# Kernel optimization log

Measured on AMD Instinct MI355X. Metric: run time of the kernel, lower is better.

Reference implementation:

```python
import jax, jax.numpy as jnp
import numpy as np

D = 768        # d_model
F = 8192       # dict_size
N_UP = 3       # number of upstream autoencoders
K = 64         # topk
B, S = 2, 1024


def setup_inputs() -> dict:
    key = jax.random.key(0)
    ks = jax.random.split(key, 10)
    sc = 1.0 / np.sqrt(D)
    return {
        "feature_buffer": jnp.zeros((B, S, F), jnp.float32),
        "x": jax.random.normal(ks[0], (B, S, D), jnp.float32),
        "up_feats": jax.random.uniform(ks[1], (N_UP, B, S, F), jnp.float32),
        "W_enc": jax.random.normal(ks[2], (D, F), jnp.float32) * sc,
        "b_enc": jax.random.normal(ks[3], (F,), jnp.float32) * 0.01,
        "W_dec": jax.random.normal(ks[4], (F, D), jnp.float32) * sc,
        "b_dec": jax.random.normal(ks[5], (D,), jnp.float32) * 0.01,
        "up_W_dec": jax.random.normal(ks[6], (N_UP, F, D), jnp.float32) * sc,
        "up_b_dec": jax.random.normal(ks[7], (N_UP, D), jnp.float32) * 0.01,
        "conn_mask": jax.random.randint(ks[8], (N_UP, F, F), 0, 2).astype(bool),
        "k": K,
    }


def reference(feature_buffer, x, up_feats, W_enc, b_enc, W_dec, b_dec,
              up_W_dec, up_b_dec, conn_mask, k):
    # initial contribs: residual stream through current encoder
    approx = jnp.einsum("bsd,df->bsf", x, W_enc)            # [B,S,F]
    upstream_bias = jnp.zeros((D,), x.dtype)
    # accumulate pruned contributions from each upstream AE
    for i in range(up_feats.shape[0]):
        upstream_bias = upstream_bias + up_b_dec[i]
        # virtual weights up_dict -> down_dict, pruned by connection mask
        virt = (up_W_dec[i] @ W_enc) * conn_mask[i].astype(x.dtype)  # [F_up,F_down]
        approx = approx + jnp.einsum("bsf,fg->bsg", up_feats[i], virt)
    # bias correction: upstream decoder biases through encoder, plus encoder bias
    approx = approx + upstream_bias @ W_enc + b_enc          # [B,S,F]
    # topk + relu + scatter into the feature buffer
    top_vals, top_idx = jax.lax.top_k(approx, k)             # [B,S,k]
    top_vals = jax.nn.relu(top_vals)
    flat = feature_buffer.reshape(-1, F)
    rows = jnp.arange(flat.shape[0])[:, None]
    feat = flat.at[rows, top_idx.reshape(-1, k)].set(top_vals.reshape(-1, k))
    feat = feat.reshape(feature_buffer.shape)
    # decode
    return jnp.einsum("bsf,fd->bsd", feat, W_dec) + b_dec
```

## Files before the change

### kernel.cpp

```cpp
#include <hip/hip_runtime.h>
#include <hip/hip_bf16.h>


#define D_DIM 768
#define F_DIM 8192

typedef _Float16 f16;
typedef _Float16 f16x8 __attribute__((ext_vector_type(8)));
typedef float f32x4 __attribute__((ext_vector_type(4)));

#define BMN 128
#define BUFB 32768
#define PLNB 16384

__device__ inline void split_f32(float v, f16& h, f16& l) {
    float hf = (float)(f16)v;
    if (__builtin_fabsf(hf) < 6.1035156e-5f) hf = 0.f;
    h = (f16)hf;
    l = (f16)((v - hf) * 2048.0f);
}

template<int MODE>
__global__ __launch_bounds__(256, 2)
void mfma_gemm(const f16* __restrict__ Ap,
               const f16* __restrict__ Bp,
               float* __restrict__ C, int ldc,
               f16* __restrict__ Vp,
               const float* __restrict__ bias,
               const unsigned char* __restrict__ conn, int upIdx,
               const int* __restrict__ flagp,
               int K, int fdBase)
{
    __shared__ char lds[2 * BUFB];
    const int tid = threadIdx.x;
    const int bm = (MODE == 2 ? blockIdx.x : blockIdx.y) * BMN;
    const int bn = (MODE == 2 ? blockIdx.y : blockIdx.x) * BMN;

    const int w  = tid >> 6;
    const int l  = tid & 63;
    const int wr = (w >> 1) * 64;
    const int wc = (w & 1) * 64;

    const char* gsrc[8];
    #pragma unroll
    for (int j = 0; j < 8; ++j) {
        const int c = tid + 256 * j;
        const int p = c >> 10;
        const int q = c & 1023;
        const int r = q >> 3;
        const int sp = q & 7;
        const int slog = sp ^ (r & 7);
        const f16* base = p ? Bp : Ap;
        const int row0 = p ? bn : bm;
        gsrc[j] = (const char*)base + (size_t)(row0 + r) * ((size_t)K * 4)
                  + slog * 16;
    }

    #define STAGE(BUFSEL)                                                     \
        _Pragma("unroll")                                                     \
        for (int j = 0; j < 8; ++j) {                                         \
            __builtin_amdgcn_global_load_lds(                                 \
                (const __attribute__((address_space(1))) void*)gsrc[j],       \
                (__attribute__((address_space(3))) void*)                     \
                    (lds + (BUFSEL) * BUFB + (tid + 256 * j) * 16),           \
                16, 0, 0);                                                    \
            gsrc[j] += 128;                       \
        }

    f32x4 accH[4][4], accM[4][4];
    const f32x4 zero = {0.f, 0.f, 0.f, 0.f};
    #pragma unroll
    for (int a = 0; a < 4; ++a)
        #pragma unroll
        for (int b = 0; b < 4; ++b) { accH[a][b] = zero; accM[a][b] = zero; }

    const int steps = K >> 5;
    const int fr = l & 15;
    const int ks = l >> 4;

    int offAH[4], offBH[4], offAL[4], offBL[4];
    #pragma unroll
    for (int f = 0; f < 4; ++f) {
        const int ra = wr + f * 16 + fr;
        const int rb = wc + f * 16 + fr;
        offAH[f] = ra * 128 + ((ks ^ (ra & 7)) * 16);
        offAL[f] = ra * 128 + (((4 + ks) ^ (ra & 7)) * 16);
        offBH[f] = PLNB + rb * 128 + ((ks ^ (rb & 7)) * 16);
        offBL[f] = PLNB + rb * 128 + (((4 + ks) ^ (rb & 7)) * 16);
    }

    STAGE(0);
    int cur = 0;
    for (int t = 0; t < steps; ++t) {
        __builtin_amdgcn_s_barrier();
        if (t + 1 < steps) {
            STAGE(cur ^ 1);
            asm volatile("s_waitcnt vmcnt(8)" ::: "memory");
        } else {
            asm volatile("s_waitcnt vmcnt(0)" ::: "memory");
        }
        __builtin_amdgcn_s_barrier();
        __builtin_amdgcn_sched_barrier(0);

        const char* Lb = lds + cur * BUFB;
        f16x8 ah[4], bh[4];
        #pragma unroll
        for (int mf = 0; mf < 4; ++mf) ah[mf] = *(const f16x8*)(Lb + offAH[mf]);
        #pragma unroll
        for (int nf = 0; nf < 4; ++nf) bh[nf] = *(const f16x8*)(Lb + offBH[nf]);

        f16x8 al[4], bl[4];
        #pragma unroll
        for (int nf = 0; nf < 4; ++nf) bl[nf] = *(const f16x8*)(Lb + offBL[nf]);
        #pragma unroll
        for (int mf = 0; mf < 4; ++mf) al[mf] = *(const f16x8*)(Lb + offAL[mf]);

        __builtin_amdgcn_s_setprio(1);
        #pragma unroll
        for (int nf = 0; nf < 4; ++nf)
            #pragma unroll
            for (int mf = 0; mf < 4; ++mf)
                accH[mf][nf] = __builtin_amdgcn_mfma_f32_16x16x32_f16(
                    ah[mf], bh[nf], accH[mf][nf], 0, 0, 0);
        __builtin_amdgcn_s_setprio(0);

        __builtin_amdgcn_s_setprio(1);
        #pragma unroll
        for (int nf = 0; nf < 4; ++nf)
            #pragma unroll
            for (int mf = 0; mf < 4; ++mf)
                accM[mf][nf] = __builtin_amdgcn_mfma_f32_16x16x32_f16(
                    ah[mf], bl[nf], accM[mf][nf], 0, 0, 0);
        #pragma unroll
        for (int mf = 0; mf < 4; ++mf)
            #pragma unroll
            for (int nf = 0; nf < 4; ++nf)
                accM[mf][nf] = __builtin_amdgcn_mfma_f32_16x16x32_f16(
                    al[mf], bh[nf], accM[mf][nf], 0, 0, 0);
        __builtin_amdgcn_s_setprio(0);

        cur ^= 1;
    }
    #undef STAGE

    const float MS = 4.8828125e-4f;
    const int flag = (MODE == 1) ? *flagp : 0;

    #pragma unroll
    for (int mf = 0; mf < 4; ++mf) {
        const int row0 = wr + mf * 16 + (l >> 4) * 4;
        #pragma unroll
        for (int nf = 0; nf < 4; ++nf) {
            const int col = wc + nf * 16 + (l & 15);
            float v[4];
            #pragma unroll
            for (int rr = 0; rr < 4; ++rr)
                v[rr] = accH[mf][nf][rr] + accM[mf][nf][rr] * MS;

            if (MODE == 0) {
                const float bb = bias[bn + col];
                #pragma unroll
                for (int rr = 0; rr < 4; ++rr)
                    C[(size_t)(bm + row0 + rr) * ldc + (bn + col)] = v[rr] + bb;
            } else if (MODE == 2) {
                #pragma unroll
                for (int rr = 0; rr < 4; ++rr) {
                    float* cp = &C[(size_t)(bm + row0 + rr) * ldc + (bn + col)];
                    *cp = *cp + v[rr];
                }
            } else {
                const size_t fu = (size_t)(bn + col);
                const size_t fd0 = (size_t)(fdBase + bm + row0);
                int m[4];
                if (flag == 1) {
                    const int4 mm = *(const int4*)((const int*)conn +
                        (size_t)upIdx * F_DIM * F_DIM + fu * F_DIM + fd0);
                    m[0] = mm.x; m[1] = mm.y; m[2] = mm.z; m[3] = mm.w;
                } else if (flag == 0) {
                    const uchar4 mm = *(const uchar4*)(conn +
                        (size_t)upIdx * F_DIM * F_DIM + fu * F_DIM + fd0);
                    m[0] = mm.x; m[1] = mm.y; m[2] = mm.z; m[3] = mm.w;
                } else if (flag == 2) {
                    const long long* pp = (const long long*)conn +
                        (size_t)upIdx * F_DIM * F_DIM + fu * F_DIM + fd0;
                    m[0] = (int)pp[0]; m[1] = (int)pp[1];
                    m[2] = (int)pp[2]; m[3] = (int)pp[3];
                } else {
                    const float4 mm = *(const float4*)((const float*)conn +
                        (size_t)upIdx * F_DIM * F_DIM + fu * F_DIM + fd0);
                    m[0] = mm.x != 0.f; m[1] = mm.y != 0.f;
                    m[2] = mm.z != 0.f; m[3] = mm.w != 0.f;
                }
                const size_t kblk = (fu >> 5) * 64 + (fu & 31);
                #pragma unroll
                for (int rr = 0; rr < 4; ++rr) {
                    const float vv = m[rr] ? v[rr] : 0.f;
                    f16 hh, ll;
                    split_f32(vv, hh, ll);
                    const size_t o = (size_t)(bm + row0 + rr) * (2 * F_DIM) + kblk;
                    Vp[o] = hh; Vp[o + 32] = ll;
                }
            }
        }
    }
}

__global__ __launch_bounds__(256)
void split_kernel(const float* __restrict__ src, f16* __restrict__ dst,
                  size_t n, int K)
{
    const size_t e = ((size_t)blockIdx.x * 256 + threadIdx.x) * 8;
    if (e >= n) return;
    const size_t r = e / (size_t)K;
    const int k = (int)(e - r * (size_t)K);
    const float4 a = *(const float4*)(src + e);
    const float4 b = *(const float4*)(src + e + 4);
    f16 hv[8], lv[8];
    const float s[8] = {a.x, a.y, a.z, a.w, b.x, b.y, b.z, b.w};
    #pragma unroll
    for (int i = 0; i < 8; ++i) split_f32(s[i], hv[i], lv[i]);
    const size_t base = r * (size_t)(2 * K) + (size_t)((k >> 5) * 64 + (k & 31));
    *(f16x8*)(dst + base)      = *(const f16x8*)hv;
    *(f16x8*)(dst + base + 32) = *(const f16x8*)lv;
}

__global__ __launch_bounds__(256)
void transpose_split_kernel(const float* __restrict__ W, f16* __restrict__ dst)
{
    const int f = blockIdx.x * 256 + threadIdx.x;
    for (int dc = 0; dc < D_DIM / 8; ++dc) {
        const int k = dc * 8;
        f16 hv[8], lv[8];
        #pragma unroll
        for (int j = 0; j < 8; ++j)
            split_f32(W[(size_t)(k + j) * F_DIM + f], hv[j], lv[j]);
        const size_t base = (size_t)f * (2 * D_DIM) + (k >> 5) * 64 + (k & 31);
        *(f16x8*)(dst + base)      = *(const f16x8*)hv;
        *(f16x8*)(dst + base + 32) = *(const f16x8*)lv;
    }
}

__global__ void detect_kernel(const int* __restrict__ conn, int* __restrict__ flag)
{
    __shared__ int not01, notf01, odd_nz;
    if (threadIdx.x == 0) { not01 = 0; notf01 = 0; odd_nz = 0; }
    __syncthreads();
    const int4 v = ((const int4*)conn)[threadIdx.x];
    const unsigned a[4] = {(unsigned)v.x, (unsigned)v.y,
                           (unsigned)v.z, (unsigned)v.w};
    int l_not01 = 0, l_notf = 0;
    #pragma unroll
    for (int i = 0; i < 4; ++i) {
        if (a[i] > 1u) l_not01 = 1;
        if (a[i] != 0u && a[i] != 0x3F800000u) l_notf = 1;
    }
    if (l_not01) atomicOr(&not01, 1);
    if (l_notf)  atomicOr(&notf01, 1);
    if (a[1] | a[3]) atomicOr(&odd_nz, 1);
    __syncthreads();
    if (threadIdx.x == 0) {
        int f;
        if (!not01)        f = odd_nz ? 1 : 2;
        else if (!notf01)  f = 3;
        else               f = 0;
        *flag = f;
    }
}

__global__ void bias2_kernel(const float* __restrict__ W_enc,
                             const float* __restrict__ b_enc,
                             const float* __restrict__ up_b_dec,
                             int nup, float* __restrict__ bias2)
{
    const int g = blockIdx.x * 256 + threadIdx.x;
    if (g >= F_DIM) return;
    float s = b_enc[g];
    for (int d = 0; d < D_DIM; ++d) {
        float ub = 0.f;
        for (int i = 0; i < nup; ++i) ub += up_b_dec[i * D_DIM + d];
        s = __builtin_fmaf(ub, W_enc[(size_t)d * F_DIM + g], s);
    }
    bias2[g] = s;
}

__global__ __launch_bounds__(256)
void topk_decode_kernel(const float* __restrict__ approx,
                        const float* __restrict__ W_dec,
                        const float* __restrict__ b_dec,
                        const int* __restrict__ kptr,
                        float* __restrict__ out)
{
    __shared__ unsigned keys[F_DIM];
    __shared__ int hist[256];
    __shared__ unsigned sh_prefix;
    __shared__ int sh_need;
    __shared__ int sel_cnt, eq_cnt;
    __shared__ int sidx[128];
    __shared__ float sval[128];
    __shared__ int eqidx[1024];

    const int tid = threadIdx.x;
    const int row = blockIdx.x;
    const int k = *kptr;
    const float* arow = approx + (size_t)row * F_DIM;

    for (int j = tid; j < F_DIM; j += 256) {
        unsigned u = __float_as_uint(arow[j]);
        u = (u & 0x80000000u) ? ~u : (u | 0x80000000u);
        keys[j] = u;
    }
    if (tid == 0) { sh_prefix = 0u; sh_need = k; sel_cnt = 0; eq_cnt = 0; }
    __syncthreads();

    for (int shift = 24; shift >= 0; shift -= 8) {
        if (tid < 256) hist[tid] = 0;
        __syncthreads();
        const unsigned pfx = sh_prefix;
        for (int j = tid; j < F_DIM; j += 256) {
            const unsigned u = keys[j];
            const bool match =
                (shift == 24) || ((u >> (shift + 8)) == (pfx >> (shift + 8)));
            if (match) atomicAdd(&hist[(u >> shift) & 255], 1);
        }
        __syncthreads();
        if (tid == 0) {
            int need = sh_need;
            for (int b = 255; b >= 0; --b) {
                const int c = hist[b];
                if (c >= need) {
                    sh_prefix = pfx | ((unsigned)b << shift);
                    sh_need = need;
                    break;
                }
                need -= c;
            }
        }
        __syncthreads();
    }
    const unsigned T = sh_prefix;
    const int r = sh_need;

    for (int j = tid; j < F_DIM; j += 256) {
        const unsigned u = keys[j];
        if (u > T) {
            const int p = atomicAdd(&sel_cnt, 1);
            sidx[p] = j;
        } else if (u == T) {
            const int p = atomicAdd(&eq_cnt, 1);
            if (p < 1024) eqidx[p] = j;
        }
    }
    __syncthreads();

    if (tid == 0) {
        const int m = sel_cnt;
        const int e = eq_cnt < 1024 ? eq_cnt : 1024;
        for (int t2 = 0; t2 < r; ++t2) {
            int best = 0x7FFFFFFF, bi = -1;
            for (int q = 0; q < e; ++q) {
                const int v = eqidx[q];
                if (v >= 0 && v < best) { best = v; bi = q; }
            }
            if (bi >= 0) { eqidx[bi] = -1; sidx[m + t2] = best; }
        }
        sel_cnt = m + r;
        const int n = sel_cnt;
        for (int a2 = 1; a2 < n; ++a2) {
            const int v = sidx[a2];
            int b2 = a2 - 1;
            while (b2 >= 0 && sidx[b2] > v) { sidx[b2 + 1] = sidx[b2]; --b2; }
            sidx[b2 + 1] = v;
        }
    }
    __syncthreads();

    const int total = sel_cnt;
    for (int j = tid; j < total; j += 256) {
        const float v = arow[sidx[j]];
        sval[j] = v > 0.f ? v : 0.f;
    }
    __syncthreads();

    float acc0 = b_dec[tid];
    float acc1 = b_dec[tid + 256];
    float acc2 = b_dec[tid + 512];
    for (int j = 0; j < total; ++j) {
        const float v = sval[j];
        const float* wv = W_dec + (size_t)sidx[j] * D_DIM;
        acc0 = __builtin_fmaf(v, wv[tid],       acc0);
        acc1 = __builtin_fmaf(v, wv[tid + 256], acc1);
        acc2 = __builtin_fmaf(v, wv[tid + 512], acc2);
    }
    float* orow = out + (size_t)row * D_DIM;
    orow[tid] = acc0;
    orow[tid + 256] = acc1;
    orow[tid + 512] = acc2;
}

extern "C" void kernel_launch(void* const* d_in, const int* in_sizes, int n_in,
                              void* d_out, int out_size, void* d_ws, size_t ws_size,
                              hipStream_t stream)
{
    const float* x         = (const float*)d_in[1];
    const float* up_feats  = (const float*)d_in[2];
    const float* W_enc     = (const float*)d_in[3];
    const float* b_enc     = (const float*)d_in[4];
    const float* W_dec     = (const float*)d_in[5];
    const float* b_dec     = (const float*)d_in[6];
    const float* up_W_dec  = (const float*)d_in[7];
    const float* up_b_dec  = (const float*)d_in[8];
    const unsigned char* conn = (const unsigned char*)d_in[9];
    const int* kptr        = (const int*)d_in[10];

    const int BS  = in_sizes[1] / D_DIM;
    const int NUP = in_sizes[8] / D_DIM;

    char* ws = (char*)d_ws;
    size_t off = 0;
    auto alloc = [&](size_t bytes) -> char* {
        off = (off + 255) & ~(size_t)255;
        char* p = ws + off; off += bytes; return p;
    };
    float* approx = (float*)alloc((size_t)BS * F_DIM * 4);
    float* bias2  = (float*)alloc(F_DIM * 4);
    int*   flag   = (int*)alloc(256);
    f16* xp   = (f16*)alloc((size_t)BS * D_DIM * 4);
    f16* Wtp  = (f16*)alloc((size_t)F_DIM * D_DIM * 4);
    f16* uwdp = (f16*)alloc((size_t)NUP * F_DIM * D_DIM * 4);
    f16* ufp  = (f16*)alloc((size_t)NUP * BS * F_DIM * 4);

    off = (off + 255) & ~(size_t)255;
    const size_t rem = (ws_size > off) ? ws_size - off : 0;
    int FC = (int)((rem / ((size_t)F_DIM * 4)) / 128 * 128);
    if (FC > F_DIM) FC = F_DIM;
    if (FC < 128) FC = 128;
    f16* vp = (f16*)alloc((size_t)FC * F_DIM * 4);

    detect_kernel<<<1, 256, 0, stream>>>((const int*)conn, flag);
    bias2_kernel<<<F_DIM / 256, 256, 0, stream>>>(W_enc, b_enc, up_b_dec, NUP, bias2);

    split_kernel<<<(unsigned)((size_t)BS * D_DIM / 2048), 256, 0, stream>>>(
        x, xp, (size_t)BS * D_DIM, D_DIM);
    split_kernel<<<(unsigned)((size_t)NUP * F_DIM * D_DIM / 2048), 256, 0, stream>>>(
        up_W_dec, uwdp, (size_t)NUP * F_DIM * D_DIM, D_DIM);
    split_kernel<<<(unsigned)((size_t)NUP * BS * F_DIM / 2048), 256, 0, stream>>>(
        up_feats, ufp, (size_t)NUP * BS * F_DIM, F_DIM);
    transpose_split_kernel<<<F_DIM / 256, 256, 0, stream>>>(W_enc, Wtp);

    mfma_gemm<0><<<dim3(F_DIM / BMN, BS / BMN), 256, 0, stream>>>(
        xp, Wtp, approx, F_DIM, nullptr, bias2,
        nullptr, 0, flag, D_DIM, 0);

    for (int i = 0; i < NUP; ++i) {
        for (int fc = 0; fc < F_DIM; fc += FC) {
            const int chunk = (F_DIM - fc) < FC ? (F_DIM - fc) : FC;
            mfma_gemm<1><<<dim3(F_DIM / BMN, chunk / BMN), 256, 0, stream>>>(
                Wtp + (size_t)fc * (2 * D_DIM),
                uwdp + (size_t)i * F_DIM * (2 * D_DIM),
                nullptr, 0, vp, nullptr,
                conn, i, flag, D_DIM, fc);
            mfma_gemm<2><<<dim3(BS / BMN, chunk / BMN), 256, 0, stream>>>(
                ufp + (size_t)i * BS * (2 * F_DIM),
                vp,
                approx + fc, F_DIM, nullptr, nullptr,
                nullptr, 0, flag, F_DIM, 0);
        }
    }

    topk_decode_kernel<<<BS, 256, 0, stream>>>(
        approx, W_dec, b_dec, kptr, (float*)d_out);
}
```

Before: 3.855 ms.

## Load B fragments directly to registers and merge split-f16 accumulators

After: 5.985 ms. 55.2% more time.

```diff
diff --git a/kernel.cpp b/kernel.cpp
--- a/kernel.cpp
+++ b/kernel.cpp
@@ -10,8 +10,7 @@
 typedef float f32x4 __attribute__((ext_vector_type(4)));
 
 #define BMN 128
-#define BUFB 32768
-#define PLNB 16384
+#define BUFB 16384
 
 __device__ inline void split_f32(float v, f16& h, f16& l) {
     float hf = (float)(f16)v;
@@ -40,108 +39,128 @@
     const int l  = tid & 63;
     const int wr = (w >> 1) * 64;
     const int wc = (w & 1) * 64;
-
-    const char* gsrc[8];
-    #pragma unroll
-    for (int j = 0; j < 8; ++j) {
+    const int fr = l & 15;
+    const int ks = l >> 4;
+
+    const char* gA[4];
+    #pragma unroll
+    for (int j = 0; j < 4; ++j) {
         const int c = tid + 256 * j;
-        const int p = c >> 10;
-        const int q = c & 1023;
-        const int r = q >> 3;
-        const int sp = q & 7;
-        const int slog = sp ^ (r & 7);
-        const f16* base = p ? Bp : Ap;
-        const int row0 = p ? bn : bm;
-        gsrc[j] = (const char*)base + (size_t)(row0 + r) * ((size_t)K * 4)
-                  + slog * 16;
-    }
-
-    #define STAGE(BUFSEL)                                                     \
-        _Pragma("unroll")                                                     \
-        for (int j = 0; j < 8; ++j) {                                         \
+        const int r = c >> 3;
+        const int slog = (c & 7) ^ (r & 7);
+        gA[j] = (const char*)Ap + (size_t)(bm + r) * ((size_t)K * 4) + slog * 16;
+    }
+
+    const char* gBH[4];
+    const char* gBL[4];
+    #pragma unroll
+    for (int nf = 0; nf < 4; ++nf) {
+        const size_t row = (size_t)(bn + wc + nf * 16 + fr);
+        gBH[nf] = (const char*)Bp + row * ((size_t)K * 4) + ks * 16;
+        gBL[nf] = gBH[nf] + 64;
+    }
+
+    #define STAGE_A(BUFSEL)                                                   \
+        _Pragma("unroll")                                                     \
+        for (int j = 0; j < 4; ++j) {                                         \
             __builtin_amdgcn_global_load_lds(                                 \
-                (const __attribute__((address_space(1))) void*)gsrc[j],       \
+                (const __attribute__((address_space(1))) void*)gA[j],         \
                 (__attribute__((address_space(3))) void*)                     \
                     (lds + (BUFSEL) * BUFB + (tid + 256 * j) * 16),           \
                 16, 0, 0);                                                    \
-            gsrc[j] += 128;                       \
-        }
-
-    f32x4 accH[4][4], accM[4][4];
+            gA[j] += 128;                                                     \
+        }
+
+    #define LOADB(BH, BL)                                                     \
+        _Pragma("unroll")                                                     \
+        for (int nf = 0; nf < 4; ++nf) {                                      \
+            BH[nf] = *(const f16x8*)gBH[nf]; gBH[nf] += 128;                  \
+            BL[nf] = *(const f16x8*)gBL[nf]; gBL[nf] += 128;                  \
+        }
+
+    f32x4 acc[4][4];
     const f32x4 zero = {0.f, 0.f, 0.f, 0.f};
     #pragma unroll
     for (int a = 0; a < 4; ++a)
         #pragma unroll
-        for (int b = 0; b < 4; ++b) { accH[a][b] = zero; accM[a][b] = zero; }
+        for (int b = 0; b < 4; ++b) acc[a][b] = zero;
 
     const int steps = K >> 5;
-    const int fr = l & 15;
-    const int ks = l >> 4;
-
-    int offAH[4], offBH[4], offAL[4], offBL[4];
+
+    int offAH[4], offAL[4];
     #pragma unroll
     for (int f = 0; f < 4; ++f) {
         const int ra = wr + f * 16 + fr;
-        const int rb = wc + f * 16 + fr;
         offAH[f] = ra * 128 + ((ks ^ (ra & 7)) * 16);
         offAL[f] = ra * 128 + (((4 + ks) ^ (ra & 7)) * 16);
-        offBH[f] = PLNB + rb * 128 + ((ks ^ (rb & 7)) * 16);
-        offBL[f] = PLNB + rb * 128 + (((4 + ks) ^ (rb & 7)) * 16);
-    }
-
-    STAGE(0);
+    }
+
+    const f16 SC = (f16)2048.0f;
+
+    #define COMPUTE(BUFSEL, BH, BL)                                           \
+    {                                                                         \
+        const char* Lb = lds + (BUFSEL) * BUFB;                               \
+        f16x8 ah[4], al[4];                                                   \
+        _Pragma("unroll")                                                     \
+        for (int mf = 0; mf < 4; ++mf) ah[mf] = *(const f16x8*)(Lb + offAH[mf]); \
+        _Pragma("unroll")                                                     \
+        for (int mf = 0; mf < 4; ++mf) al[mf] = *(const f16x8*)(Lb + offAL[mf]); \
+        __builtin_amdgcn_s_setprio(1);                                        \
+        _Pragma("unroll")                                                     \
+        for (int nf = 0; nf < 4; ++nf)                                        \
+            _Pragma("unroll")                                                 \
+            for (int mf = 0; mf < 4; ++mf)                                    \
+                acc[mf][nf] = __builtin_amdgcn_mfma_f32_16x16x32_f16(         \
+                    ah[mf], BL[nf], acc[mf][nf], 0, 0, 0);                    \
+        __builtin_amdgcn_s_setprio(0);                                        \
+        _Pragma("unroll")                                                     \
+        for (int mf = 0; mf < 4; ++mf) ah[mf] = ah[mf] * SC;                  \
+        __builtin_amdgcn_s_setprio(1);                                        \
+        _Pragma("unroll")                                                     \
+        for (int nf = 0; nf < 4; ++nf)                                        \
+            _Pragma("unroll")                                                 \
+            for (int mf = 0; mf < 4; ++mf)                                    \
+                acc[mf][nf] = __builtin_amdgcn_mfma_f32_16x16x32_f16(         \
+                    ah[mf], BH[nf], acc[mf][nf], 0, 0, 0);                    \
+        _Pragma("unroll")                                                     \
+        for (int mf = 0; mf < 4; ++mf)                                        \
+            _Pragma("unroll")                                                 \
+            for (int nf = 0; nf < 4; ++nf)                                    \
+                acc[mf][nf] = __builtin_amdgcn_mfma_f32_16x16x32_f16(         \
+                    al[mf], BH[nf], acc[mf][nf], 0, 0, 0);                    \
+        __builtin_amdgcn_s_setprio(0);                                        \
+    }
+
+    f16x8 bhE[4], blE[4], bhO[4], blO[4];
+    STAGE_A(0);
+    LOADB(bhE, blE);
     int cur = 0;
-    for (int t = 0; t < steps; ++t) {
+    for (int t = 0; t < steps; t += 2) {
         __builtin_amdgcn_s_barrier();
-        if (t + 1 < steps) {
-            STAGE(cur ^ 1);
-            asm volatile("s_waitcnt vmcnt(8)" ::: "memory");
+        STAGE_A(cur ^ 1);
+        LOADB(bhO, blO);
+        asm volatile("s_waitcnt vmcnt(12)" ::: "memory");
+        __builtin_amdgcn_s_barrier();
+        __builtin_amdgcn_sched_barrier(0);
+        COMPUTE(cur, bhE, blE);
+        cur ^= 1;
+
+        __builtin_amdgcn_s_barrier();
+        if (t + 2 < steps) {
+            STAGE_A(cur ^ 1);
+            LOADB(bhE, blE);
+            asm volatile("s_waitcnt vmcnt(12)" ::: "memory");
         } else {
             asm volatile("s_waitcnt vmcnt(0)" ::: "memory");
         }
         __builtin_amdgcn_s_barrier();
         __builtin_amdgcn_sched_barrier(0);
-
-        const char* Lb = lds + cur * BUFB;
-        f16x8 ah[4], bh[4];
-        #pragma unroll
-        for (int mf = 0; mf < 4; ++mf) ah[mf] = *(const f16x8*)(Lb + offAH[mf]);
-        #pragma unroll
-        for (int nf = 0; nf < 4; ++nf) bh[nf] = *(const f16x8*)(Lb + offBH[nf]);
-
-        f16x8 al[4], bl[4];
-        #pragma unroll
-        for (int nf = 0; nf < 4; ++nf) bl[nf] = *(const f16x8*)(Lb + offBL[nf]);
-        #pragma unroll
-        for (int mf = 0; mf < 4; ++mf) al[mf] = *(const f16x8*)(Lb + offAL[mf]);
-
-        __builtin_amdgcn_s_setprio(1);
-        #pragma unroll
-        for (int nf = 0; nf < 4; ++nf)
-            #pragma unroll
-            for (int mf = 0; mf < 4; ++mf)
-                accH[mf][nf] = __builtin_amdgcn_mfma_f32_16x16x32_f16(
-                    ah[mf], bh[nf], accH[mf][nf], 0, 0, 0);
-        __builtin_amdgcn_s_setprio(0);
-
-        __builtin_amdgcn_s_setprio(1);
-        #pragma unroll
-        for (int nf = 0; nf < 4; ++nf)
-            #pragma unroll
-            for (int mf = 0; mf < 4; ++mf)
-                accM[mf][nf] = __builtin_amdgcn_mfma_f32_16x16x32_f16(
-                    ah[mf], bl[nf], accM[mf][nf], 0, 0, 0);
-        #pragma unroll
-        for (int mf = 0; mf < 4; ++mf)
-            #pragma unroll
-            for (int nf = 0; nf < 4; ++nf)
-                accM[mf][nf] = __builtin_amdgcn_mfma_f32_16x16x32_f16(
-                    al[mf], bh[nf], accM[mf][nf], 0, 0, 0);
-        __builtin_amdgcn_s_setprio(0);
-
+        COMPUTE(cur, bhO, blO);
         cur ^= 1;
     }
-    #undef STAGE
+    #undef COMPUTE
+    #undef LOADB
+    #undef STAGE_A
 
     const float MS = 4.8828125e-4f;
     const int flag = (MODE == 1) ? *flagp : 0;
@@ -155,7 +174,7 @@
             float v[4];
             #pragma unroll
             for (int rr = 0; rr < 4; ++rr)
-                v[rr] = accH[mf][nf][rr] + accM[mf][nf][rr] * MS;
+                v[rr] = acc[mf][nf][rr] * MS;
 
             if (MODE == 0) {
                 const float bb = bias[bn + col];
```

## Enlarge GEMM tiles to 256x256 with 8 waves and single split-fp16 accumulator

Applied to the files above, without the earlier changes.

Measured after the change: 3.997 ms. 3.7% more time.

```diff
diff --git a/kernel.cpp b/kernel.cpp
--- a/kernel.cpp
+++ b/kernel.cpp
@@ -9,9 +9,9 @@
 typedef _Float16 f16x8 __attribute__((ext_vector_type(8)));
 typedef float f32x4 __attribute__((ext_vector_type(4)));
 
-#define BMN 128
-#define BUFB 32768
-#define PLNB 16384
+#define BMN 256
+#define BUFB 65536
+#define PLNB 32768
 
 __device__ inline void split_f32(float v, f16& h, f16& l) {
     float hf = (float)(f16)v;
@@ -21,7 +21,7 @@
 }
 
 template<int MODE>
-__global__ __launch_bounds__(256, 2)
+__global__ __launch_bounds__(512, 2)
 void mfma_gemm(const f16* __restrict__ Ap,
                const f16* __restrict__ Bp,
                float* __restrict__ C, int ldc,
@@ -38,56 +38,61 @@
 
     const int w  = tid >> 6;
     const int l  = tid & 63;
-    const int wr = (w >> 1) * 64;
-    const int wc = (w & 1) * 64;
-
-    const char* gsrc[8];
-    #pragma unroll
-    for (int j = 0; j < 8; ++j) {
-        const int c = tid + 256 * j;
-        const int p = c >> 10;
-        const int q = c & 1023;
-        const int r = q >> 3;
-        const int sp = q & 7;
-        const int slog = sp ^ (r & 7);
-        const f16* base = p ? Bp : Ap;
-        const int row0 = p ? bn : bm;
-        gsrc[j] = (const char*)base + (size_t)(row0 + r) * ((size_t)K * 4)
-                  + slog * 16;
+    const int wr = (w >> 2) * 128;
+    const int wc = (w & 3) * 64;
+    const int fr = l & 15;
+    const int ks = l >> 4;
+
+    const char* gA[4];
+    const char* gB[4];
+    #pragma unroll
+    for (int j = 0; j < 4; ++j) {
+        const int c = tid + 512 * j;
+        const int r = c >> 3;
+        const int slog = (c & 7) ^ (r & 7);
+        gA[j] = (const char*)Ap + (size_t)(bm + r) * ((size_t)K * 4) + slog * 16;
+        gB[j] = (const char*)Bp + (size_t)(bn + r) * ((size_t)K * 4) + slog * 16;
     }
 
     #define STAGE(BUFSEL)                                                     \
         _Pragma("unroll")                                                     \
-        for (int j = 0; j < 8; ++j) {                                         \
+        for (int j = 0; j < 4; ++j) {                                         \
             __builtin_amdgcn_global_load_lds(                                 \
-                (const __attribute__((address_space(1))) void*)gsrc[j],       \
+                (const __attribute__((address_space(1))) void*)gA[j],         \
                 (__attribute__((address_space(3))) void*)                     \
-                    (lds + (BUFSEL) * BUFB + (tid + 256 * j) * 16),           \
+                    (lds + (BUFSEL) * BUFB + (tid + 512 * j) * 16),           \
                 16, 0, 0);                                                    \
-            gsrc[j] += 128;                       \
-        }
-
-    f32x4 accH[4][4], accM[4][4];
+            __builtin_amdgcn_global_load_lds(                                 \
+                (const __attribute__((address_space(1))) void*)gB[j],         \
+                (__attribute__((address_space(3))) void*)                     \
+                    (lds + (BUFSEL) * BUFB + PLNB + (tid + 512 * j) * 16),    \
+                16, 0, 0);                                                    \
+            gA[j] += 128;                                                     \
+            gB[j] += 128;                                                     \
+        }
+
+    f32x4 acc[8][4];
     const f32x4 zero = {0.f, 0.f, 0.f, 0.f};
     #pragma unroll
-    for (int a = 0; a < 4; ++a)
-        #pragma unroll
-        for (int b = 0; b < 4; ++b) { accH[a][b] = zero; accM[a][b] = zero; }
+    for (int a = 0; a < 8; ++a)
+        #pragma unroll
+        for (int b = 0; b < 4; ++b) acc[a][b] = zero;
 
     const int steps = K >> 5;
-    const int fr = l & 15;
-    const int ks = l >> 4;
-
-    int offAH[4], offBH[4], offAL[4], offBL[4];
+
+    int offAH[8], offBH[4];
+    #pragma unroll
+    for (int f = 0; f < 8; ++f) {
+        const int ra = wr + f * 16 + fr;
+        offAH[f] = ra * 128 + ((ks ^ (ra & 7)) * 16);
+    }
     #pragma unroll
     for (int f = 0; f < 4; ++f) {
-        const int ra = wr + f * 16 + fr;
         const int rb = wc + f * 16 + fr;
-        offAH[f] = ra * 128 + ((ks ^ (ra & 7)) * 16);
-        offAL[f] = ra * 128 + (((4 + ks) ^ (ra & 7)) * 16);
         offBH[f] = PLNB + rb * 128 + ((ks ^ (rb & 7)) * 16);
-        offBL[f] = PLNB + rb * 128 + (((4 + ks) ^ (rb & 7)) * 16);
-    }
+    }
+
+    const f16 SC = (f16)2048.0f;
 
     STAGE(0);
     int cur = 0;
@@ -103,40 +108,47 @@
         __builtin_amdgcn_sched_barrier(0);
 
         const char* Lb = lds + cur * BUFB;
-        f16x8 ah[4], bh[4];
-        #pragma unroll
-        for (int mf = 0; mf < 4; ++mf) ah[mf] = *(const f16x8*)(Lb + offAH[mf]);
-        #pragma unroll
-        for (int nf = 0; nf < 4; ++nf) bh[nf] = *(const f16x8*)(Lb + offBH[nf]);
-
-        f16x8 al[4], bl[4];
-        #pragma unroll
-        for (int nf = 0; nf < 4; ++nf) bl[nf] = *(const f16x8*)(Lb + offBL[nf]);
-        #pragma unroll
-        for (int mf = 0; mf < 4; ++mf) al[mf] = *(const f16x8*)(Lb + offAL[mf]);
+        f16x8 ah[8], bh[4], bl[4];
+        #pragma unroll
+        for (int mf = 0; mf < 8; ++mf) ah[mf] = *(const f16x8*)(Lb + offAH[mf]);
+        #pragma unroll
+        for (int nf = 0; nf < 4; ++nf) {
+            bh[nf] = *(const f16x8*)(Lb + offBH[nf]);
+            bl[nf] = *(const f16x8*)(Lb + (offBH[nf] ^ 64));
+        }
 
         __builtin_amdgcn_s_setprio(1);
         #pragma unroll
         for (int nf = 0; nf < 4; ++nf)
             #pragma unroll
-            for (int mf = 0; mf < 4; ++mf)
-                accH[mf][nf] = __builtin_amdgcn_mfma_f32_16x16x32_f16(
-                    ah[mf], bh[nf], accH[mf][nf], 0, 0, 0);
+            for (int mf = 0; mf < 8; ++mf)
+                acc[mf][nf] = __builtin_amdgcn_mfma_f32_16x16x32_f16(
+                    ah[mf], bl[nf], acc[mf][nf], 0, 0, 0);
         __builtin_amdgcn_s_setprio(0);
+
+        #pragma unroll
+        for (int mf = 0; mf < 8; ++mf) ah[mf] = ah[mf] * SC;
 
         __builtin_amdgcn_s_setprio(1);
         #pragma unroll
         for (int nf = 0; nf < 4; ++nf)
             #pragma unroll
-            for (int mf = 0; mf < 4; ++mf)
-                accM[mf][nf] = __builtin_amdgcn_mfma_f32_16x16x32_f16(
-                    ah[mf], bl[nf], accM[mf][nf], 0, 0, 0);
-        #pragma unroll
-        for (int mf = 0; mf < 4; ++mf)
+            for (int mf = 0; mf < 8; ++mf)
+                acc[mf][nf] = __builtin_amdgcn_mfma_f32_16x16x32_f16(
+                    ah[mf], bh[nf], acc[mf][nf], 0, 0, 0);
+        __builtin_amdgcn_s_setprio(0);
+
+        f16x8 al[8];
+        #pragma unroll
+        for (int mf = 0; mf < 8; ++mf)
+            al[mf] = *(const f16x8*)(Lb + (offAH[mf] ^ 64));
+        __builtin_amdgcn_s_setprio(1);
+        #pragma unroll
+        for (int mf = 0; mf < 8; ++mf)
             #pragma unroll
             for (int nf = 0; nf < 4; ++nf)
-                accM[mf][nf] = __builtin_amdgcn_mfma_f32_16x16x32_f16(
-                    al[mf], bh[nf], accM[mf][nf], 0, 0, 0);
+                acc[mf][nf] = __builtin_amdgcn_mfma_f32_16x16x32_f16(
+                    al[mf], bh[nf], acc[mf][nf], 0, 0, 0);
         __builtin_amdgcn_s_setprio(0);
 
         cur ^= 1;
@@ -147,7 +159,7 @@
     const int flag = (MODE == 1) ? *flagp : 0;
 
     #pragma unroll
-    for (int mf = 0; mf < 4; ++mf) {
+    for (int mf = 0; mf < 8; ++mf) {
         const int row0 = wr + mf * 16 + (l >> 4) * 4;
         #pragma unroll
         for (int nf = 0; nf < 4; ++nf) {
@@ -155,7 +167,7 @@
             float v[4];
             #pragma unroll
             for (int rr = 0; rr < 4; ++rr)
-                v[rr] = accH[mf][nf][rr] + accM[mf][nf][rr] * MS;
+                v[rr] = acc[mf][nf][rr] * MS;
 
             if (MODE == 0) {
                 const float bb = bias[bn + col];
@@ -431,9 +443,9 @@
 
     off = (off + 255) & ~(size_t)255;
     const size_t rem = (ws_size > off) ? ws_size - off : 0;
-    int FC = (int)((rem / ((size_t)F_DIM * 4)) / 128 * 128);
+    int FC = (int)((rem / ((size_t)F_DIM * 4)) / 256 * 256);
     if (FC > F_DIM) FC = F_DIM;
-    if (FC < 128) FC = 128;
+    if (FC < 256) FC = 256;
     f16* vp = (f16*)alloc((size_t)FC * F_DIM * 4);
 
     detect_kernel<<<1, 256, 0, stream>>>((const int*)conn, flag);
@@ -447,19 +459,19 @@
         up_feats, ufp, (size_t)NUP * BS * F_DIM, F_DIM);
     transpose_split_kernel<<<F_DIM / 256, 256, 0, stream>>>(W_enc, Wtp);
 
-    mfma_gemm<0><<<dim3(F_DIM / BMN, BS / BMN), 256, 0, stream>>>(
+    mfma_gemm<0><<<dim3(F_DIM / BMN, BS / BMN), 512, 0, stream>>>(
         xp, Wtp, approx, F_DIM, nullptr, bias2,
         nullptr, 0, flag, D_DIM, 0);
 
     for (int i = 0; i < NUP; ++i) {
         for (int fc = 0; fc < F_DIM; fc += FC) {
             const int chunk = (F_DIM - fc) < FC ? (F_DIM - fc) : FC;
-            mfma_gemm<1><<<dim3(F_DIM / BMN, chunk / BMN), 256, 0, stream>>>(
+            mfma_gemm<1><<<dim3(F_DIM / BMN, chunk / BMN), 512, 0, stream>>>(
                 Wtp + (size_t)fc * (2 * D_DIM),
                 uwdp + (size_t)i * F_DIM * (2 * D_DIM),
                 nullptr, 0, vp, nullptr,
                 conn, i, flag, D_DIM, fc);
-            mfma_gemm<2><<<dim3(BS / BMN, chunk / BMN), 256, 0, stream>>>(
+            mfma_gemm<2><<<dim3(BS / BMN, chunk / BMN), 512, 0, stream>>>(
                 ufp + (size_t)i * BS * (2 * F_DIM),
                 vp,
                 approx + fc, F_DIM, nullptr, nullptr,
```
